# Kernel optimization log

Measured on AMD Instinct MI355X. Metric: run time of the kernel, lower is better.

Reference implementation:

```python
import jax, jax.numpy as jnp
import numpy as np

B, S, D, H = 2, 4096, 1024, 16
DK = D // H


def setup_inputs() -> dict:
    key = jax.random.key(0)
    ks = jax.random.split(key, 7)
    sc = 1.0 / np.sqrt(D)
    return {
        "q": jax.random.normal(ks[0], (B, S, D), jnp.float32),
        "k": jax.random.normal(ks[1], (B, S, D), jnp.float32),
        "v": jax.random.normal(ks[2], (B, S, D), jnp.float32),
        "wq": jax.random.normal(ks[3], (D, D), jnp.float32) * sc,
        "wk": jax.random.normal(ks[4], (D, D), jnp.float32) * sc,
        "wv": jax.random.normal(ks[5], (D, D), jnp.float32) * sc,
        "w0": jax.random.normal(ks[6], (D, D), jnp.float32) * sc,
    }


def reference(q, k, v, wq, wk, wv, w0):
    # Linear(bias=False): y = x @ W^T  (torch convention, W is [out,in])
    qp = jnp.einsum('bsd,ed->bse', q, wq).reshape(B, S, H, DK).transpose(0, 2, 1, 3)
    kp = jnp.einsum('bsd,ed->bse', k, wk).reshape(B, S, H, DK).transpose(0, 2, 1, 3)
    vp = jnp.einsum('bsd,ed->bse', v, wv).reshape(B, S, H, DK).transpose(0, 2, 1, 3)
    scale = 1.0 / jnp.sqrt(jnp.float32(DK))
    att = jnp.einsum('bhqd,bhkd->bhqk', qp, kp) * scale  # [B,H,S,S]
    att = jax.nn.softmax(att, axis=-1)
    x = jnp.einsum('bhqk,bhkd->bhqd', att, vp)  # [B,H,S,DK]
    x = x.transpose(0, 2, 1, 3).reshape(B, S, D)
    out = jnp.einsum('bsd,ed->bse', x, w0)
    return out
```

## Files before the change

kernel.cpp:

```cpp
#include <hip/hip_runtime.h>
#include <hip/hip_bf16.h>
#include <stdint.h>

#define Bb 2
#define Ss 4096
#define Dd 1024
#define Hh 16
#define DKk 64

typedef __attribute__((ext_vector_type(8))) short bf16x8;
typedef __attribute__((ext_vector_type(4))) float f32x4;
typedef __attribute__((ext_vector_type(16))) float f32x16;

#define MFMA16(a, b, c) __builtin_amdgcn_mfma_f32_32x32x16_bf16(a, b, c, 0, 0, 0)

__device__ __forceinline__ unsigned short f2bf(float f) {
    union { float f; unsigned int u; } x; x.f = f;
    return (unsigned short)((x.u + 0x7fffu + ((x.u >> 16) & 1u)) >> 16);
}

__device__ __forceinline__ void gload16(const void* g, void* l) {
    __builtin_amdgcn_global_load_lds(
        (const __attribute__((address_space(1))) void*)g,
        (__attribute__((address_space(3))) void*)l, 16, 0, 0);
}

__global__ __launch_bounds__(256) void cvt_all(const float* __restrict__ q, const float* __restrict__ k,
                                               const float* __restrict__ v, const float* __restrict__ wq,
                                               const float* __restrict__ wk, const float* __restrict__ wv,
                                               const float* __restrict__ w0, unsigned short* __restrict__ ws) {
    const int QKV4 = 3 * 2097152;
    const int TOT4 = QKV4 + 4 * 262144;
    int i = blockIdx.x * 256 + threadIdx.x;
    const int stride = gridDim.x * 256;
    ushort4* out = (ushort4*)ws;
    for (; i < TOT4; i += stride) {
        const float4* src;
        int di;
        if (i < QKV4) {
            const int r = i >> 21;
            const float* s = r == 0 ? q : (r == 1 ? k : v);
            src = (const float4*)s + (i & 2097151);
            di = i;
        } else {
            const int j = i - QKV4;
            const int r = j >> 18;
            const float* s = r == 0 ? wq : (r == 1 ? wk : (r == 2 ? wv : w0));
            src = (const float4*)s + (j & 262143);
            di = i + 2097152;
        }
        const float4 vv = *src;
        ushort4 o;
        o.x = f2bf(vv.x); o.y = f2bf(vv.y); o.z = f2bf(vv.z); o.w = f2bf(vv.w);
        out[di] = o;
    }
}

template <int MODE>
__global__ __launch_bounds__(256) void gemm_bt(const unsigned short* __restrict__ A,
                                               const unsigned short* __restrict__ W,
                                               void* __restrict__ Y) {
    __shared__ unsigned short As[128 * 32];
    __shared__ unsigned short Bs[128 * 32];
    const int t = threadIdx.x;
    const int wid = t >> 6, lane = t & 63, q4 = lane >> 4, l16 = lane & 15;
    const int wr = wid >> 1, wc = wid & 1;
    const int arow0 = blockIdx.x * 128;
    const int wrow0 = blockIdx.y * 128;
    f32x4 acc[4][4] = {};
    for (int kt = 0; kt < 1024; kt += 32) {
        __syncthreads();
#pragma unroll
        for (int i = 0; i < 2; i++) {
            const int o = i * 4096 + t * 16;
            const int r = o >> 6, c = (o & 63) >> 1;
            gload16(A + (long)(arow0 + r) * 1024 + kt + c, (char*)As + o);
            gload16(W + (long)(wrow0 + r) * 1024 + kt + c, (char*)Bs + o);
        }
        __syncthreads();
        bf16x8 a[4], b[4];
#pragma unroll
        for (int m = 0; m < 4; m++)
            a[m] = *(const bf16x8*)((const char*)As + (wr * 64 + m * 16 + l16) * 64 + q4 * 16);
#pragma unroll
        for (int n = 0; n < 4; n++)
            b[n] = *(const bf16x8*)((const char*)Bs + (wc * 64 + n * 16 + l16) * 64 + q4 * 16);
#pragma unroll
        for (int m = 0; m < 4; m++)
#pragma unroll
            for (int n = 0; n < 4; n++)
                acc[m][n] = __builtin_amdgcn_mfma_f32_16x16x32_bf16(a[m], b[n], acc[m][n], 0, 0, 0);
    }
    const int rb = arow0 + wr * 64, cb = wrow0 + wc * 64;
#pragma unroll
    for (int m = 0; m < 4; m++)
#pragma unroll
        for (int n = 0; n < 4; n++)
#pragma unroll
            for (int r = 0; r < 4; r++) {
                const int row = rb + m * 16 + q4 * 4 + r;
                const int col = cb + n * 16 + l16;
                const float v = acc[m][n][r];
                if (MODE == 0) {
                    ((unsigned short*)Y)[(long)row * 1024 + col] = f2bf(v);
                } else if (MODE == 1) {
                    const int bb = row >> 12, s = row & 4095;
                    const int hh = col >> 6, dk = col & 63;
                    ((unsigned short*)Y)[(((long)(bb * Hh + hh) * DKk + dk) << 12) + s] = f2bf(v);
                } else if (MODE == 3) {
                    ((unsigned short*)Y)[(long)row * 1024 + col] = f2bf(v * 0.1803368801111244f);
                } else {
                    ((float*)Y)[(long)row * 1024 + col] = v;
                }
            }
}

__global__ __launch_bounds__(512, 4) void attn_fwd(const unsigned short* __restrict__ qp,
                                                   const unsigned short* __restrict__ kp,
                                                   const unsigned short* __restrict__ vt,
                                                   unsigned short* __restrict__ xo) {
    __shared__ __align__(16) char smem[32768];
    const int t = threadIdx.x;
    const int wid = t >> 6, lane = t & 63;
    const int l5 = lane & 31;
    const int ihi = lane >> 5;
    const int swz5 = (l5 & 7) ^ ((l5 >> 3) & 3);
    const int qt = blockIdx.x, h = blockIdx.y, b = blockIdx.z;
    const unsigned short* qbase = qp + ((long)b * Ss + qt * 256) * Dd + h * 64;
    const unsigned short* kbase = kp + (long)b * Ss * Dd + h * 64;
    const unsigned short* vbase = vt + (long)(b * Hh + h) * DKk * Ss;

    const int r0 = t >> 3;
    const int s0i = t & 7;
    const int cb0 = s0i ^ (r0 & 7) ^ ((r0 >> 3) & 3);
    const int o0 = t * 16;
    const unsigned short* qsrc = qbase + (long)r0 * Dd + cb0 * 8;
    const unsigned short* ksrc = kbase + (long)r0 * Dd + cb0 * 8;
    const unsigned short* vsrc = vbase + (long)r0 * Ss + cb0 * 8;

#pragma unroll
    for (int i = 0; i < 4; i++)
        gload16(qsrc + (long)i * 64 * Dd, smem + i * 8192 + o0);
    asm volatile("s_waitcnt vmcnt(0)" ::: "memory");
    __builtin_amdgcn_s_barrier();
    asm volatile("" ::: "memory");

    bf16x8 bQ[4];
#pragma unroll
    for (int m = 0; m < 4; m++) {
        const int slot = (m * 2 + ihi) ^ swz5;
        bQ[m] = *(const bf16x8*)(smem + wid * 4096 + l5 * 128 + (slot << 4));
    }
    asm volatile("s_waitcnt lgkmcnt(0)" ::: "memory");
    __builtin_amdgcn_s_barrier();
    asm volatile("" ::: "memory");

    gload16(ksrc,                smem + o0);
    gload16(vsrc,                smem + 8192 + o0);
    gload16(ksrc + 64 * Dd,      smem + 16384 + o0);
    gload16(vsrc + 64,           smem + 24576 + o0);
    const unsigned short* pk = ksrc + 128 * Dd;
    const unsigned short* pv = vsrc + 128;
    asm volatile("s_waitcnt vmcnt(2)" ::: "memory");
    __builtin_amdgcn_s_barrier();
    asm volatile("" ::: "memory");

    int adm[4];
#pragma unroll
    for (int m = 0; m < 4; m++)
        adm[m] = l5 * 128 + ((((m * 2 + ihi) ^ swz5)) << 4);

    f32x16 accO[2] = {};
    float li = 0.f;

    for (int kt2 = 0; kt2 < 64; kt2 += 2) {
#pragma unroll
        for (int hf = 0; hf < 2; hf++) {
            const int kt = kt2 + hf;
            const int BO = hf << 14;
            const char* Kc = smem + BO;
            const char* Vc = smem + BO + 8192;
            f32x16 accS[2] = {};
            __builtin_amdgcn_s_setprio(1);
#pragma unroll
            for (int m = 0; m < 4; m++) {
                const bf16x8 aK0 = *(const bf16x8*)(Kc + adm[m]);
                const bf16x8 aK1 = *(const bf16x8*)(Kc + 4096 + adm[m]);
                accS[0] = MFMA16(aK0, bQ[m], accS[0]);
                accS[1] = MFMA16(aK1, bQ[m], accS[1]);
            }
            float ps = 0.f;
#pragma unroll
            for (int m = 0; m < 4; m++) {
                const bf16x8 aV0 = *(const bf16x8*)(Vc + adm[m]);
                const bf16x8 aV1 = *(const bf16x8*)(Vc + 4096 + adm[m]);
                const int kb = m >> 1, sx = (m & 1) * 2;
                unsigned w00, w01, w10, w11;
                {
                    const float a0 = __builtin_amdgcn_exp2f(accS[kb][4 * sx + 0]);
                    const float a1 = __builtin_amdgcn_exp2f(accS[kb][4 * sx + 1]);
                    const float a2 = __builtin_amdgcn_exp2f(accS[kb][4 * sx + 2]);
                    const float a3 = __builtin_amdgcn_exp2f(accS[kb][4 * sx + 3]);
                    const float b0 = __builtin_amdgcn_exp2f(accS[kb][4 * sx + 4]);
                    const float b1 = __builtin_amdgcn_exp2f(accS[kb][4 * sx + 5]);
                    const float b2 = __builtin_amdgcn_exp2f(accS[kb][4 * sx + 6]);
                    const float b3 = __builtin_amdgcn_exp2f(accS[kb][4 * sx + 7]);
                    ps += ((a0 + a1) + (a2 + a3)) + ((b0 + b1) + (b2 + b3));
                    asm("v_cvt_pk_bf16_f32 %0, %1, %2" : "=v"(w00) : "v"(a0), "v"(a1));
                    asm("v_cvt_pk_bf16_f32 %0, %1, %2" : "=v"(w01) : "v"(a2), "v"(a3));
                    asm("v_cvt_pk_bf16_f32 %0, %1, %2" : "=v"(w10) : "v"(b0), "v"(b1));
                    asm("v_cvt_pk_bf16_f32 %0, %1, %2" : "=v"(w11) : "v"(b2), "v"(b3));
                }
                asm("v_permlane32_swap_b32 %0, %1" : "+v"(w00), "+v"(w10));
                asm("v_permlane32_swap_b32 %0, %1" : "+v"(w01), "+v"(w11));
                union { unsigned u[4]; bf16x8 v; } fr;
                fr.u[0] = w00; fr.u[1] = w01; fr.u[2] = w10; fr.u[3] = w11;
                accO[0] = MFMA16(aV0, fr.v, accO[0]);
                accO[1] = MFMA16(aV1, fr.v, accO[1]);
            }
            __builtin_amdgcn_s_setprio(0);
            li += ps + __shfl_xor(ps, 32, 64);
            __builtin_amdgcn_s_barrier();
            asm volatile("" ::: "memory");
            if (kt < 62) {
                char* dst = smem + BO;
                gload16(pk, dst + o0);
                gload16(pv, dst + 8192 + o0);
                pk += 64 * Dd;
                pv += 64;
                asm volatile("s_waitcnt vmcnt(2)" ::: "memory");
            } else {
                asm volatile("s_waitcnt vmcnt(0)" ::: "memory");
            }
            __builtin_amdgcn_s_barrier();
            asm volatile("" ::: "memory");
        }
    }

    const float rli = 1.0f / li;
#pragma unroll
    for (int dblk = 0; dblk < 2; dblk++)
#pragma unroll
        for (int tt = 0; tt < 8; tt++) {
            const unsigned short b0 = f2bf(accO[dblk][2 * tt] * rli);
            const unsigned short b1 = f2bf(accO[dblk][2 * tt + 1] * rli);
            const int slot = (dblk * 4 + (tt >> 1)) ^ swz5;
            const int phys = wid * 4096 + l5 * 128 + (slot << 4) + ihi * 8 + (tt & 1) * 4;
            *(unsigned*)(smem + phys) = ((unsigned)b1 << 16) | b0;
        }
    __syncthreads();
#pragma unroll
    for (int p = 0; p < 4; p++) {
        const uint4 val = *(const uint4*)(smem + p * 8192 + o0);
        const long row = (long)qt * 256 + p * 64 + r0;
        *(uint4*)(xo + ((long)b * Ss + row) * Dd + h * 64 + cb0 * 8) = val;
    }
}

extern "C" void kernel_launch(void* const* d_in, const int* in_sizes, int n_in,
                              void* d_out, int out_size, void* d_ws, size_t ws_size,
                              hipStream_t stream) {
    const float* q  = (const float*)d_in[0];
    const float* k  = (const float*)d_in[1];
    const float* v  = (const float*)d_in[2];
    const float* wq = (const float*)d_in[3];
    const float* wk = (const float*)d_in[4];
    const float* wv = (const float*)d_in[5];
    const float* w0 = (const float*)d_in[6];

    unsigned short* ws = (unsigned short*)d_ws;
    const long NE = (long)Bb * Ss * Dd;
    unsigned short* qb  = ws;
    unsigned short* kb  = ws + NE;
    unsigned short* vb  = ws + 2 * NE;
    unsigned short* x1  = ws + 3 * NE;
    unsigned short* wqb = ws + 4 * NE;
    unsigned short* wkb = wqb + 1048576;
    unsigned short* wvb = wkb + 1048576;
    unsigned short* w0b = wvb + 1048576;

    cvt_all<<<2048, 256, 0, stream>>>(q, k, v, wq, wk, wv, w0, ws);

    dim3 gg(64, 8);
    gemm_bt<3><<<gg, 256, 0, stream>>>(qb, wqb, x1);
    gemm_bt<0><<<gg, 256, 0, stream>>>(kb, wkb, qb);
    gemm_bt<1><<<gg, 256, 0, stream>>>(vb, wvb, kb);
    dim3 ga(16, 16, 2);
    attn_fwd<<<ga, 512, 0, stream>>>(x1, qb, kb, vb);
    gemm_bt<2><<<gg, 256, 0, stream>>>(vb, w0b, (float*)d_out);
}
```

Before: 268.1 us.

## Double-buffer LDS tiles in projection GEMM with async global-to-LDS prefetch

Turns the bt GEMM's single-buffered LDS tiles into a two-stage ping-pong buffer. The tile two steps ahead is prefetched with global_load_lds while the current tile feeds the MFMAs, using manual vmcnt waits and raw barriers in place of __syncthreads. This is meant to hide global load latency in the QKV and output projections. It doubles LDS use per block, and the hand-written waitcnt and barrier ordering could hide a race if the counts are wrong.

```diff
diff --git a/kernel.cpp b/kernel.cpp
--- a/kernel.cpp
+++ b/kernel.cpp
@@ -60,37 +60,63 @@
 __global__ __launch_bounds__(256) void gemm_bt(const unsigned short* __restrict__ A,
                                                const unsigned short* __restrict__ W,
                                                void* __restrict__ Y) {
-    __shared__ unsigned short As[128 * 32];
-    __shared__ unsigned short Bs[128 * 32];
+    __shared__ unsigned short As[2][128 * 32];
+    __shared__ unsigned short Bs[2][128 * 32];
     const int t = threadIdx.x;
     const int wid = t >> 6, lane = t & 63, q4 = lane >> 4, l16 = lane & 15;
     const int wr = wid >> 1, wc = wid & 1;
     const int arow0 = blockIdx.x * 128;
     const int wrow0 = blockIdx.y * 128;
+    const int o0 = t * 16, o1 = 4096 + t * 16;
+    const int r0 = o0 >> 6, c0 = (o0 & 63) >> 1;
+    const int r1 = o1 >> 6, c1 = (o1 & 63) >> 1;
+    const unsigned short* a0 = A + (long)(arow0 + r0) * 1024 + c0;
+    const unsigned short* a1 = A + (long)(arow0 + r1) * 1024 + c1;
+    const unsigned short* w0p = W + (long)(wrow0 + r0) * 1024 + c0;
+    const unsigned short* w1p = W + (long)(wrow0 + r1) * 1024 + c1;
+
+#pragma unroll
+    for (int i = 0; i < 2; i++) {
+        gload16(a0 + i * 32,  (char*)As[i] + o0);
+        gload16(a1 + i * 32,  (char*)As[i] + o1);
+        gload16(w0p + i * 32, (char*)Bs[i] + o0);
+        gload16(w1p + i * 32, (char*)Bs[i] + o1);
+    }
+    asm volatile("s_waitcnt vmcnt(4)" ::: "memory");
+    __builtin_amdgcn_s_barrier();
+    asm volatile("" ::: "memory");
+
     f32x4 acc[4][4] = {};
-    for (int kt = 0; kt < 1024; kt += 32) {
-        __syncthreads();
-#pragma unroll
-        for (int i = 0; i < 2; i++) {
-            const int o = i * 4096 + t * 16;
-            const int r = o >> 6, c = (o & 63) >> 1;
-            gload16(A + (long)(arow0 + r) * 1024 + kt + c, (char*)As + o);
-            gload16(W + (long)(wrow0 + r) * 1024 + kt + c, (char*)Bs + o);
-        }
-        __syncthreads();
+    for (int kt = 0; kt < 32; kt++) {
+        const int buf = kt & 1;
         bf16x8 a[4], b[4];
 #pragma unroll
         for (int m = 0; m < 4; m++)
-            a[m] = *(const bf16x8*)((const char*)As + (wr * 64 + m * 16 + l16) * 64 + q4 * 16);
+            a[m] = *(const bf16x8*)((const char*)As[buf] + (wr * 64 + m * 16 + l16) * 64 + q4 * 16);
 #pragma unroll
         for (int n = 0; n < 4; n++)
-            b[n] = *(const bf16x8*)((const char*)Bs + (wc * 64 + n * 16 + l16) * 64 + q4 * 16);
+            b[n] = *(const bf16x8*)((const char*)Bs[buf] + (wc * 64 + n * 16 + l16) * 64 + q4 * 16);
 #pragma unroll
         for (int m = 0; m < 4; m++)
 #pragma unroll
             for (int n = 0; n < 4; n++)
                 acc[m][n] = __builtin_amdgcn_mfma_f32_16x16x32_bf16(a[m], b[n], acc[m][n], 0, 0, 0);
-    }
+        __builtin_amdgcn_s_barrier();
+        asm volatile("" ::: "memory");
+        if (kt < 30) {
+            const int kc = (kt + 2) * 32;
+            gload16(a0 + kc,  (char*)As[buf] + o0);
+            gload16(a1 + kc,  (char*)As[buf] + o1);
+            gload16(w0p + kc, (char*)Bs[buf] + o0);
+            gload16(w1p + kc, (char*)Bs[buf] + o1);
+            asm volatile("s_waitcnt vmcnt(4)" ::: "memory");
+        } else {
+            asm volatile("s_waitcnt vmcnt(0)" ::: "memory");
+        }
+        __builtin_amdgcn_s_barrier();
+        asm volatile("" ::: "memory");
+    }
+
     const int rb = arow0 + wr * 64, cb = wrow0 + wc * 64;
 #pragma unroll
     for (int m = 0; m < 4; m++)
```

Result: no change. 270.8 us (+1.0%).

## Fuse fp32-to-bf16 activation conversion into projection GEMM A-tile loads

Applied to the files above, without the earlier changes.

The standalone pass that converted q/k/v activations to bf16 is removed. The projection GEMMs now read fp32 activations directly, prefetch the next K-slice into registers, and pack them to bf16 with v_cvt_pk_bf16_f32 before storing to LDS. Only the weights still go through a separate conversion kernel. This avoids a full write and re-read of bf16 copies of q/k/v, but the GEMMs now read twice as many bytes for A, use register-staged LDS stores instead of direct global-to-LDS loads, and A tiles are re-read once per column block.

```diff
diff --git a/kernel.cpp b/kernel.cpp
--- a/kernel.cpp
+++ b/kernel.cpp
@@ -25,39 +25,20 @@
         (__attribute__((address_space(3))) void*)l, 16, 0, 0);
 }
 
-__global__ __launch_bounds__(256) void cvt_all(const float* __restrict__ q, const float* __restrict__ k,
-                                               const float* __restrict__ v, const float* __restrict__ wq,
-                                               const float* __restrict__ wk, const float* __restrict__ wv,
-                                               const float* __restrict__ w0, unsigned short* __restrict__ ws) {
-    const int QKV4 = 3 * 2097152;
-    const int TOT4 = QKV4 + 4 * 262144;
-    int i = blockIdx.x * 256 + threadIdx.x;
-    const int stride = gridDim.x * 256;
-    ushort4* out = (ushort4*)ws;
-    for (; i < TOT4; i += stride) {
-        const float4* src;
-        int di;
-        if (i < QKV4) {
-            const int r = i >> 21;
-            const float* s = r == 0 ? q : (r == 1 ? k : v);
-            src = (const float4*)s + (i & 2097151);
-            di = i;
-        } else {
-            const int j = i - QKV4;
-            const int r = j >> 18;
-            const float* s = r == 0 ? wq : (r == 1 ? wk : (r == 2 ? wv : w0));
-            src = (const float4*)s + (j & 262143);
-            di = i + 2097152;
-        }
-        const float4 vv = *src;
-        ushort4 o;
-        o.x = f2bf(vv.x); o.y = f2bf(vv.y); o.z = f2bf(vv.z); o.w = f2bf(vv.w);
-        out[di] = o;
-    }
-}
-
-template <int MODE>
-__global__ __launch_bounds__(256) void gemm_bt(const unsigned short* __restrict__ A,
+__global__ __launch_bounds__(256) void cvt_w(const float* __restrict__ wq, const float* __restrict__ wk,
+                                             const float* __restrict__ wv, const float* __restrict__ w0,
+                                             unsigned short* __restrict__ dst) {
+    const int i = blockIdx.x * 256 + threadIdx.x;
+    const int r = i >> 18, j = i & 262143;
+    const float* s = r == 0 ? wq : (r == 1 ? wk : (r == 2 ? wv : w0));
+    const float4 v = ((const float4*)s)[j];
+    ushort4 o;
+    o.x = f2bf(v.x); o.y = f2bf(v.y); o.z = f2bf(v.z); o.w = f2bf(v.w);
+    ((ushort4*)dst)[i] = o;
+}
+
+template <int MODE, int AF32>
+__global__ __launch_bounds__(256) void gemm_bt(const void* __restrict__ Av,
                                                const unsigned short* __restrict__ W,
                                                void* __restrict__ Y) {
     __shared__ unsigned short As[128 * 32];
@@ -67,17 +48,49 @@
     const int wr = wid >> 1, wc = wid & 1;
     const int arow0 = blockIdx.x * 128;
     const int wrow0 = blockIdx.y * 128;
+    const int o0 = t * 16, o1 = 4096 + t * 16;
+    const unsigned short* Ab = (const unsigned short*)Av;
+    const int r0 = o0 >> 6, c0 = (o0 & 63) >> 1;
+    const int r1 = o1 >> 6, c1 = (o1 & 63) >> 1;
+    const float* Af = (const float*)Av;
+    const int ar = t >> 1, ac = (t & 1) * 16;
+    const float* aptr = Af + (long)(arow0 + ar) * 1024 + ac;
+    const int adst = ar * 64 + (t & 1) * 32;
+
+    float4 pf0, pf1, pf2, pf3;
+    if (AF32) {
+        const float4* p = (const float4*)aptr;
+        pf0 = p[0]; pf1 = p[1]; pf2 = p[2]; pf3 = p[3];
+    }
+
     f32x4 acc[4][4] = {};
-    for (int kt = 0; kt < 1024; kt += 32) {
+    for (int kt = 0; kt < 32; kt++) {
         __syncthreads();
-#pragma unroll
-        for (int i = 0; i < 2; i++) {
-            const int o = i * 4096 + t * 16;
-            const int r = o >> 6, c = (o & 63) >> 1;
-            gload16(A + (long)(arow0 + r) * 1024 + kt + c, (char*)As + o);
-            gload16(W + (long)(wrow0 + r) * 1024 + kt + c, (char*)Bs + o);
+        if (AF32) {
+            unsigned w[8];
+            asm("v_cvt_pk_bf16_f32 %0, %1, %2" : "=v"(w[0]) : "v"(pf0.x), "v"(pf0.y));
+            asm("v_cvt_pk_bf16_f32 %0, %1, %2" : "=v"(w[1]) : "v"(pf0.z), "v"(pf0.w));
+            asm("v_cvt_pk_bf16_f32 %0, %1, %2" : "=v"(w[2]) : "v"(pf1.x), "v"(pf1.y));
+            asm("v_cvt_pk_bf16_f32 %0, %1, %2" : "=v"(w[3]) : "v"(pf1.z), "v"(pf1.w));
+            asm("v_cvt_pk_bf16_f32 %0, %1, %2" : "=v"(w[4]) : "v"(pf2.x), "v"(pf2.y));
+            asm("v_cvt_pk_bf16_f32 %0, %1, %2" : "=v"(w[5]) : "v"(pf2.z), "v"(pf2.w));
+            asm("v_cvt_pk_bf16_f32 %0, %1, %2" : "=v"(w[6]) : "v"(pf3.x), "v"(pf3.y));
+            asm("v_cvt_pk_bf16_f32 %0, %1, %2" : "=v"(w[7]) : "v"(pf3.z), "v"(pf3.w));
+            uint4 d0 = make_uint4(w[0], w[1], w[2], w[3]);
+            uint4 d1 = make_uint4(w[4], w[5], w[6], w[7]);
+            *(uint4*)((char*)As + adst) = d0;
+            *(uint4*)((char*)As + adst + 16) = d1;
+        } else {
+            gload16(Ab + (long)(arow0 + r0) * 1024 + kt * 32 + c0, (char*)As + o0);
+            gload16(Ab + (long)(arow0 + r1) * 1024 + kt * 32 + c1, (char*)As + o1);
         }
+        gload16(W + (long)(wrow0 + r0) * 1024 + kt * 32 + c0, (char*)Bs + o0);
+        gload16(W + (long)(wrow0 + r1) * 1024 + kt * 32 + c1, (char*)Bs + o1);
         __syncthreads();
+        if (AF32 && kt < 31) {
+            const float4* p = (const float4*)(aptr + (kt + 1) * 32);
+            pf0 = p[0]; pf1 = p[1]; pf2 = p[2]; pf3 = p[3];
+        }
         bf16x8 a[4], b[4];
 #pragma unroll
         for (int m = 0; m < 4; m++)
@@ -91,6 +104,7 @@
             for (int n = 0; n < 4; n++)
                 acc[m][n] = __builtin_amdgcn_mfma_f32_16x16x32_bf16(a[m], b[n], acc[m][n], 0, 0, 0);
     }
+
     const int rb = arow0 + wr * 64, cb = wrow0 + wc * 64;
 #pragma unroll
     for (int m = 0; m < 4; m++)
@@ -270,22 +284,22 @@
 
     unsigned short* ws = (unsigned short*)d_ws;
     const long NE = (long)Bb * Ss * Dd;
-    unsigned short* qb  = ws;
-    unsigned short* kb  = ws + NE;
-    unsigned short* vb  = ws + 2 * NE;
+    unsigned short* kp  = ws;
+    unsigned short* vt  = ws + NE;
+    unsigned short* xo  = ws + 2 * NE;
     unsigned short* x1  = ws + 3 * NE;
     unsigned short* wqb = ws + 4 * NE;
     unsigned short* wkb = wqb + 1048576;
     unsigned short* wvb = wkb + 1048576;
     unsigned short* w0b = wvb + 1048576;
 
-    cvt_all<<<2048, 256, 0, stream>>>(q, k, v, wq, wk, wv, w0, ws);
+    cvt_w<<<4096, 256, 0, stream>>>(wq, wk, wv, w0, wqb);
 
     dim3 gg(64, 8);
-    gemm_bt<3><<<gg, 256, 0, stream>>>(qb, wqb, x1);
-    gemm_bt<0><<<gg, 256, 0, stream>>>(kb, wkb, qb);
-    gemm_bt<1><<<gg, 256, 0, stream>>>(vb, wvb, kb);
+    gemm_bt<3, 1><<<gg, 256, 0, stream>>>(q, wqb, x1);
+    gemm_bt<0, 1><<<gg, 256, 0, stream>>>(k, wkb, kp);
+    gemm_bt<1, 1><<<gg, 256, 0, stream>>>(v, wvb, vt);
     dim3 ga(16, 16, 2);
-    attn_fwd<<<ga, 512, 0, stream>>>(x1, qb, kb, vb);
-    gemm_bt<2><<<gg, 256, 0, stream>>>(vb, w0b, (float*)d_out);
-}
+    attn_fwd<<<ga, 512, 0, stream>>>(x1, kp, vt, xo);
+    gemm_bt<2, 0><<<gg, 256, 0, stream>>>(xo, w0b, (float*)d_out);
+}
```

After: 282.1 us. +5.2%, slower.
